# Optimization experiments

Measured on AMD Instinct MI355X. Metric: run time of the kernel, lower is better.

Reference implementation:

```python
import jax, jax.numpy as jnp
import numpy as np

N_BINS = 15
DELTA = 1.0 / N_BINS


def setup_inputs() -> dict:
    key = jax.random.key(0)
    k1, k2 = jax.random.split(key)
    N, C = 4_000_000, 10
    # scale 5 -> confident softmax -> low collision entropy so bins [0,1) are populated
    logits = jax.random.normal(k1, (N, C), dtype=jnp.float32) * 5.0
    labels = jax.random.randint(k2, (N,), 0, C)
    return {"logits": logits, "labels": labels}


def reference(logits, labels):
    # probs: [N, C]
    probs = jax.nn.softmax(logits, axis=-1)
    # collision entropy H2 per sample: [N]
    u = -jnp.log2(jnp.sum(probs * probs, axis=-1) + 1e-12)
    err_real = (jnp.argmax(probs, axis=-1) != labels).astype(jnp.float32)  # [N]

    n = u.shape[0]
    # bin b covers [b*DELTA, (b+1)*DELTA); samples with u outside [0,1) go to overflow bin
    bin_idx = jnp.floor(u / DELTA).astype(jnp.int32)
    valid = (u >= 0.0) & (u < 1.0)
    seg = jnp.where(valid, bin_idx, N_BINS)

    vf = valid.astype(jnp.float32)
    counts = jax.ops.segment_sum(vf, seg, num_segments=N_BINS + 1)[:N_BINS]
    sum_u = jax.ops.segment_sum(jnp.where(valid, u, 0.0), seg, num_segments=N_BINS + 1)[:N_BINS]
    sum_err = jax.ops.segment_sum(jnp.where(valid, err_real, 0.0), seg, num_segments=N_BINS + 1)[:N_BINS]

    pi = counts / n                      # population weight per bin
    nonempty = counts > 0
    cnt = jnp.where(nonempty, counts, 1.0)
    u_b = sum_u / cnt                    # mean H2 in bin
    err_b = sum_err / cnt                # empirical error rate in bin

    # risk-from-H2 reference curve
    inner = jnp.clip(2.0 * jnp.exp2(-u_b) - 1.0, 0.0, None)
    r_ref = 0.5 * (1.0 - jnp.sqrt(inner))

    gaps = jnp.where(nonempty, jnp.abs(err_b - r_ref) * pi, 0.0)
    return jnp.sum(gaps)
```

## Files before the change

### kernel.cpp

```cpp
#include <hip/hip_runtime.h>
#include <math.h>
#include <stdint.h>

#define NB 15
#define TROWS 512
#define TBYTES (TROWS * 40)
#define NCOPY 8
#define ACCSTRIDE 64


__device__ __forceinline__ void gload_lds16(const void* g, float* ldsBase, uint32_t ldsByteOff)
{
    __builtin_amdgcn_global_load_lds(
        (const __attribute__((address_space(1))) uint32_t*)g,
        (__attribute__((address_space(3))) uint32_t*)((char*)ldsBase + ldsByteOff),
        16, 0, 0);
}

__device__ __forceinline__ void row_stats(const float lv[10], float lvl_lab, bool rowOK,
                                          int& bin, float& u, int& e10)
{
    float m = lv[0];
#pragma unroll
    for (int j = 1; j < 10; ++j) m = fmaxf(m, lv[j]);

    const float c = 1.44269504088896340736f;
    float mc = m * c;
    float Z = 0.0f, S = 0.0f;
#pragma unroll
    for (int j = 0; j < 10; ++j) {
        float e = exp2f(fmaf(lv[j], c, -mc));
        Z += e;
        S = fmaf(e, e, S);
    }
    float ratio = S * __builtin_amdgcn_rcpf(Z * Z);
    u = -log2f(ratio + 1e-12f);

    bool valid = rowOK && (u >= 0.0f) && (u < 1.0f);
    bin = -1;
    if (valid) {
        bin = (int)(u * 15.0f);
        if (bin > 14) bin = 14;
    }
    if (!valid) u = 0.0f;
    e10 = (lvl_lab != m) ? 1 : 0;
}

__global__ __launch_bounds__(256) void bin_kernel(
    const float* __restrict__ logits,
    const int* __restrict__ labels,
    float* __restrict__ acc,
    int N, int numTiles)
{
    __shared__ float lds[TROWS * 10];
    __shared__ float s_acc[3 * NB];

    const int t = threadIdx.x;
    if (t < 3 * NB) s_acc[t] = 0.0f;
    const int wid  = t >> 6;
    const int lane = t & 63;

    int   pk[NB];
    float su[NB];
#pragma unroll
    for (int b = 0; b < NB; ++b) { pk[b] = 0; su[b] = 0.0f; }

    const char* srcB = (const char*)logits;
    const long long totB = (long long)N * 40;

    for (int tile = blockIdx.x; tile < numTiles; tile += gridDim.x) {
        const long long tb = (long long)tile * TBYTES;

        const int r0 = tile * TROWS + t;
        const int r1 = r0 + 256;
        const int lab0 = (r0 < N) ? labels[r0] : 0;
        const int lab1 = (r1 < N) ? labels[r1] : 0;

        __syncthreads();
#pragma unroll
        for (int k = 0; k < 5; ++k) {
            uint32_t loff = (uint32_t)(wid * 5 + k) << 10;
            long long gb = tb + loff + lane * 16;
            if (gb < totB)
                gload_lds16(srcB + gb, lds, __builtin_amdgcn_readfirstlane(loff));
        }
        __syncthreads();

        float a[10], b2[10];
        {
            const float2* p = (const float2*)(lds + t * 10);
#pragma unroll
            for (int j = 0; j < 5; ++j) { float2 w = p[j]; a[2*j] = w.x; a[2*j+1] = w.y; }
        }
        {
            const float2* p = (const float2*)(lds + (t + 256) * 10);
#pragma unroll
            for (int j = 0; j < 5; ++j) { float2 w = p[j]; b2[2*j] = w.x; b2[2*j+1] = w.y; }
        }
        float lvl0 = lds[t * 10 + lab0];
        float lvl1 = lds[(t + 256) * 10 + lab1];

        int binA, eA, binB, eB;
        float uA, uB;
        row_stats(a,  lvl0, r0 < N, binA, uA, eA);
        row_stats(b2, lvl1, r1 < N, binB, uB, eB);

        int incA = 1 + (eA << 16);
        int incB = 1 + (eB << 16);
#pragma unroll
        for (int b = 0; b < NB; ++b) {
            bool mA = (binA == b);
            bool mB = (binB == b);
            pk[b] += (mA ? incA : 0) + (mB ? incB : 0);
            su[b] += (mA ? uA : 0.0f) + (mB ? uB : 0.0f);
        }
    }

#pragma unroll
    for (int b = 0; b < NB; ++b) {
        int   p = pk[b];
        float s = su[b];
#pragma unroll
        for (int off = 1; off < 64; off <<= 1) {
            p += __shfl_xor(p, off, 64);
            s += __shfl_xor(s, off, 64);
        }
        if (lane == 0) {
            atomicAdd(&s_acc[b],          (float)(p & 0xFFFF));
            atomicAdd(&s_acc[NB + b],     s);
            atomicAdd(&s_acc[2 * NB + b], (float)(p >> 16));
        }
    }
    __syncthreads();
    if (t < 3 * NB) {
        float v = s_acc[t];
        if (v != 0.0f)
            atomicAdd(&acc[(blockIdx.x & (NCOPY - 1)) * ACCSTRIDE + t], v);
    }
}

__global__ void finalize_kernel(const float* __restrict__ acc,
                                float* __restrict__ out, float n)
{
    int b = threadIdx.x;
    float gap = 0.0f;
    if (b < NB) {
        float cnt = 0.0f, sumu = 0.0f, serr = 0.0f;
#pragma unroll
        for (int c = 0; c < NCOPY; ++c) {
            cnt  += acc[c * ACCSTRIDE + b];
            sumu += acc[c * ACCSTRIDE + NB + b];
            serr += acc[c * ACCSTRIDE + 2 * NB + b];
        }
        if (cnt > 0.0f) {
            float u_b   = sumu / cnt;
            float err_b = serr / cnt;
            float inner = 2.0f * exp2f(-u_b) - 1.0f;
            if (inner < 0.0f) inner = 0.0f;
            float r_ref = 0.5f * (1.0f - sqrtf(inner));
            gap = fabsf(err_b - r_ref) * (cnt / n);
        }
    }
#pragma unroll
    for (int off = 32; off >= 1; off >>= 1)
        gap += __shfl_xor(gap, off, 64);
    if (b == 0) out[0] = gap;
}

extern "C" void kernel_launch(void* const* d_in, const int* in_sizes, int n_in,
                              void* d_out, int out_size, void* d_ws, size_t ws_size,
                              hipStream_t stream)
{
    const float* logits = (const float*)d_in[0];
    const int*   labels = (const int*)d_in[1];
    const int N = in_sizes[1];

    float* acc = (float*)d_ws;
    hipMemsetAsync(acc, 0, NCOPY * ACCSTRIDE * sizeof(float), stream);

    const int numTiles = (N + TROWS - 1) / TROWS;
    int blocks = numTiles < 1792 ? numTiles : 1792;
    bin_kernel<<<blocks, 256, 0, stream>>>(logits, labels, acc, N, numTiles);
    finalize_kernel<<<1, 64, 0, stream>>>(acc, (float*)d_out, (float)N);
}
```

Measured before the change: 245.9 us.

## Double-buffer LDS tile loads and pack per-bin counters into nibbles

Adds a two-buffer LDS pipeline: the async global-to-LDS load for the next tile is issued before computing the current tile, and the label for the next tile is prefetched. This hides load latency and leaves one barrier per iteration. Tiles shrink to 256 rows, so each thread handles one row per iteration. The 15 packed int accumulators are replaced by four nibble-packed registers for counts and errors, which cuts register pressure. The catch is that each thread must see at most 15 rows per bin, which holds only while tiles per block stay below 16.

Result: no change. 248.5 us (+1.0%).

```diff
diff --git a/kernel.cpp b/kernel.cpp
--- a/kernel.cpp
+++ b/kernel.cpp
@@ -3,7 +3,7 @@
 #include <stdint.h>
 
 #define NB 15
-#define TROWS 512
+#define TROWS 256
 #define TBYTES (TROWS * 40)
 #define NCOPY 8
 #define ACCSTRIDE 64
@@ -17,42 +17,13 @@
         16, 0, 0);
 }
 
-__device__ __forceinline__ void row_stats(const float lv[10], float lvl_lab, bool rowOK,
-                                          int& bin, float& u, int& e10)
-{
-    float m = lv[0];
-#pragma unroll
-    for (int j = 1; j < 10; ++j) m = fmaxf(m, lv[j]);
-
-    const float c = 1.44269504088896340736f;
-    float mc = m * c;
-    float Z = 0.0f, S = 0.0f;
-#pragma unroll
-    for (int j = 0; j < 10; ++j) {
-        float e = exp2f(fmaf(lv[j], c, -mc));
-        Z += e;
-        S = fmaf(e, e, S);
-    }
-    float ratio = S * __builtin_amdgcn_rcpf(Z * Z);
-    u = -log2f(ratio + 1e-12f);
-
-    bool valid = rowOK && (u >= 0.0f) && (u < 1.0f);
-    bin = -1;
-    if (valid) {
-        bin = (int)(u * 15.0f);
-        if (bin > 14) bin = 14;
-    }
-    if (!valid) u = 0.0f;
-    e10 = (lvl_lab != m) ? 1 : 0;
-}
-
 __global__ __launch_bounds__(256) void bin_kernel(
     const float* __restrict__ logits,
     const int* __restrict__ labels,
     float* __restrict__ acc,
     int N, int numTiles)
 {
-    __shared__ float lds[TROWS * 10];
+    __shared__ float lds[2][TROWS * 10];
     __shared__ float s_acc[3 * NB];
 
     const int t = threadIdx.x;
@@ -60,65 +31,108 @@
     const int wid  = t >> 6;
     const int lane = t & 63;
 
-    int   pk[NB];
+    unsigned cnt01 = 0, cnt89 = 0, err01 = 0, err89 = 0;
     float su[NB];
 #pragma unroll
-    for (int b = 0; b < NB; ++b) { pk[b] = 0; su[b] = 0.0f; }
+    for (int b = 0; b < NB; ++b) su[b] = 0.0f;
 
     const char* srcB = (const char*)logits;
     const long long totB = (long long)N * 40;
+    const int k0 = wid, k1 = wid + 4, k2 = wid + 8;
 
-    for (int tile = blockIdx.x; tile < numTiles; tile += gridDim.x) {
+    int tile = blockIdx.x;
+    {
         const long long tb = (long long)tile * TBYTES;
+        long long gb0 = tb + (k0 << 10) + lane * 16;
+        long long gb1 = tb + (k1 << 10) + lane * 16;
+        if (gb0 < totB) gload_lds16(srcB + gb0, (float*)lds, __builtin_amdgcn_readfirstlane((uint32_t)(k0 << 10)));
+        if (gb1 < totB) gload_lds16(srcB + gb1, (float*)lds, __builtin_amdgcn_readfirstlane((uint32_t)(k1 << 10)));
+        if (k2 < 10) {
+            long long gb2 = tb + (k2 << 10) + lane * 16;
+            if (gb2 < totB) gload_lds16(srcB + gb2, (float*)lds, __builtin_amdgcn_readfirstlane((uint32_t)(k2 << 10)));
+        }
+    }
+    int r0 = tile * TROWS + t;
+    int labCur = (r0 < N) ? labels[r0] : 0;
 
-        const int r0 = tile * TROWS + t;
-        const int r1 = r0 + 256;
-        const int lab0 = (r0 < N) ? labels[r0] : 0;
-        const int lab1 = (r1 < N) ? labels[r1] : 0;
+    int cur = 0;
+    for (; tile < numTiles; tile += gridDim.x) {
+        const int nxt = tile + gridDim.x;
 
         __syncthreads();
+
+        int labNext = 0;
+        if (nxt < numTiles) {
+            const long long tb = (long long)nxt * TBYTES;
+            const uint32_t bufOff = (uint32_t)((cur ^ 1) * TBYTES);
+            long long gb0 = tb + (k0 << 10) + lane * 16;
+            long long gb1 = tb + (k1 << 10) + lane * 16;
+            if (gb0 < totB) gload_lds16(srcB + gb0, (float*)lds, __builtin_amdgcn_readfirstlane(bufOff + (k0 << 10)));
+            if (gb1 < totB) gload_lds16(srcB + gb1, (float*)lds, __builtin_amdgcn_readfirstlane(bufOff + (k1 << 10)));
+            if (k2 < 10) {
+                long long gb2 = tb + (k2 << 10) + lane * 16;
+                if (gb2 < totB) gload_lds16(srcB + gb2, (float*)lds, __builtin_amdgcn_readfirstlane(bufOff + (k2 << 10)));
+            }
+            int rn = nxt * TROWS + t;
+            labNext = (rn < N) ? labels[rn] : 0;
+        }
+
+        const int r = tile * TROWS + t;
+        const bool rowOK = (r < N);
+        const float* rp = lds[cur] + t * 10;
+        float lv[10];
+        {
+            const float2* p2 = (const float2*)rp;
 #pragma unroll
-        for (int k = 0; k < 5; ++k) {
-            uint32_t loff = (uint32_t)(wid * 5 + k) << 10;
-            long long gb = tb + loff + lane * 16;
-            if (gb < totB)
-                gload_lds16(srcB + gb, lds, __builtin_amdgcn_readfirstlane(loff));
+            for (int j = 0; j < 5; ++j) { float2 w = p2[j]; lv[2*j] = w.x; lv[2*j+1] = w.y; }
         }
-        __syncthreads();
+        float m = lv[0];
+#pragma unroll
+        for (int j = 1; j < 10; ++j) m = fmaxf(m, lv[j]);
 
-        float a[10], b2[10];
-        {
-            const float2* p = (const float2*)(lds + t * 10);
+        const float c = 1.44269504088896340736f;
+        float mc = m * c;
+        float Z = 0.0f, S = 0.0f;
 #pragma unroll
-            for (int j = 0; j < 5; ++j) { float2 w = p[j]; a[2*j] = w.x; a[2*j+1] = w.y; }
+        for (int j = 0; j < 10; ++j) {
+            float e = exp2f(fmaf(lv[j], c, -mc));
+            Z += e;
+            S = fmaf(e, e, S);
         }
-        {
-            const float2* p = (const float2*)(lds + (t + 256) * 10);
+        float ratio = S * __builtin_amdgcn_rcpf(Z * Z);
+        float u = -log2f(ratio + 1e-12f);
+
+        bool valid = rowOK && (u >= 0.0f) && (u < 1.0f);
+        int bin = -1;
+        if (valid) {
+            bin = (int)(u * 15.0f);
+            if (bin > 14) bin = 14;
+        }
+        float uu = valid ? u : 0.0f;
+
+        float lvl = rp[labCur];
+        bool e10 = (lvl != m);
+
+        unsigned nib = valid ? (1u << ((bin & 7) << 2)) : 0u;
+        bool lo = ((unsigned)bin < 8u);
+        cnt01 += lo ? nib : 0u;
+        cnt89 += lo ? 0u : nib;
+        unsigned en = e10 ? nib : 0u;
+        err01 += lo ? en : 0u;
+        err89 += lo ? 0u : en;
 #pragma unroll
-            for (int j = 0; j < 5; ++j) { float2 w = p[j]; b2[2*j] = w.x; b2[2*j+1] = w.y; }
-        }
-        float lvl0 = lds[t * 10 + lab0];
-        float lvl1 = lds[(t + 256) * 10 + lab1];
+        for (int b = 0; b < NB; ++b)
+            su[b] += (bin == b) ? uu : 0.0f;
 
-        int binA, eA, binB, eB;
-        float uA, uB;
-        row_stats(a,  lvl0, r0 < N, binA, uA, eA);
-        row_stats(b2, lvl1, r1 < N, binB, uB, eB);
-
-        int incA = 1 + (eA << 16);
-        int incB = 1 + (eB << 16);
-#pragma unroll
-        for (int b = 0; b < NB; ++b) {
-            bool mA = (binA == b);
-            bool mB = (binB == b);
-            pk[b] += (mA ? incA : 0) + (mB ? incB : 0);
-            su[b] += (mA ? uA : 0.0f) + (mB ? uB : 0.0f);
-        }
+        cur ^= 1;
+        labCur = labNext;
     }
 
 #pragma unroll
     for (int b = 0; b < NB; ++b) {
-        int   p = pk[b];
+        unsigned c4 = (b < 8) ? (cnt01 >> (b * 4)) : (cnt89 >> ((b - 8) * 4));
+        unsigned e4 = (b < 8) ? (err01 >> (b * 4)) : (err89 >> ((b - 8) * 4));
+        int   p = (int)((c4 & 15u) | ((e4 & 15u) << 16));
         float s = su[b];
 #pragma unroll
         for (int off = 1; off < 64; off <<= 1) {
@@ -128,7 +142,7 @@
         if (lane == 0) {
             atomicAdd(&s_acc[b],          (float)(p & 0xFFFF));
             atomicAdd(&s_acc[NB + b],     s);
-            atomicAdd(&s_acc[2 * NB + b], (float)(p >> 16));
+            atomicAdd(&s_acc[2 * NB + b], (float)((unsigned)p >> 16));
         }
     }
     __syncthreads();
```

## Double-buffer per-wave LDS DMA microtiles and pack bin counters into nibbles

Applied to the files above, without the earlier changes.

Replaces the block-wide tile loop, which needed two __syncthreads per tile, with independent per-wave 128-row microtiles. Each wave alternates between two LDS buffers: it issues the async global-to-LDS load and the label load for a later microtile while it computes on the current one. Bin counts and error counts now use 4-bit nibble counters in packed registers, and the grid is sized so each wave handles at most 15 microtiles, which keeps the nibbles from overflowing. The aim is to hide memory latency and cut synchronisation cost. In exchange, correctness depends on the compiler inserting the right vmcnt waits before LDS reads, and tails are handled with clamped loads.

Measured after the change: 246.5 us. About the same (+0.3%).

```diff
diff --git a/kernel.cpp b/kernel.cpp
--- a/kernel.cpp
+++ b/kernel.cpp
@@ -3,27 +3,48 @@
 #include <stdint.h>
 
 #define NB 15
-#define TROWS 512
-#define TBYTES (TROWS * 40)
 #define NCOPY 8
 #define ACCSTRIDE 64
 
 
-__device__ __forceinline__ void gload_lds16(const void* g, float* ldsBase, uint32_t ldsByteOff)
+__device__ __forceinline__ void dma16(const char* g, float* ldsArr, uint32_t byteOff)
 {
     __builtin_amdgcn_global_load_lds(
         (const __attribute__((address_space(1))) uint32_t*)g,
-        (__attribute__((address_space(3))) uint32_t*)((char*)ldsBase + ldsByteOff),
+        (__attribute__((address_space(3))) uint32_t*)((char*)ldsArr + byteOff),
         16, 0, 0);
 }
 
-__device__ __forceinline__ void row_stats(const float lv[10], float lvl_lab, bool rowOK,
-                                          int& bin, float& u, int& e10)
+__device__ __forceinline__ void stage_mt(const char* srcB, long long clampHi,
+                                         float* ldsArr, uint32_t segOff,
+                                         long long mClamped, int lane)
+{
+    long long g0 = mClamped * 5120 + (long long)lane * 16;
+#pragma unroll
+    for (int c = 0; c < 5; ++c) {
+        long long g = g0 + c * 1024;
+        g = (g > clampHi) ? clampHi : g;
+        dma16(srcB + g, ldsArr, segOff + (uint32_t)(c * 1024));
+    }
+}
+
+__device__ __forceinline__ void load_labs(const int* __restrict__ labels, long long mClamped,
+                                          int lane, int N, int& la0, int& la1)
+{
+    long long r0 = mClamped * 128 + lane;
+    long long r1 = r0 + 64;
+    r0 = (r0 < N) ? r0 : (N - 1);
+    r1 = (r1 < N) ? r1 : (N - 1);
+    la0 = labels[r0];
+    la1 = labels[r1];
+}
+
+__device__ __forceinline__ void row_math(const float lv[10], float lvl, bool rowOK,
+                                         int& bin, float& uu, bool& e10)
 {
     float m = lv[0];
 #pragma unroll
     for (int j = 1; j < 10; ++j) m = fmaxf(m, lv[j]);
-
     const float c = 1.44269504088896340736f;
     float mc = m * c;
     float Z = 0.0f, S = 0.0f;
@@ -34,91 +55,131 @@
         S = fmaf(e, e, S);
     }
     float ratio = S * __builtin_amdgcn_rcpf(Z * Z);
-    u = -log2f(ratio + 1e-12f);
-
+    float u = -log2f(ratio + 1e-12f);
     bool valid = rowOK && (u >= 0.0f) && (u < 1.0f);
     bin = -1;
     if (valid) {
         bin = (int)(u * 15.0f);
         if (bin > 14) bin = 14;
     }
-    if (!valid) u = 0.0f;
-    e10 = (lvl_lab != m) ? 1 : 0;
+    uu = valid ? u : 0.0f;
+    e10 = (lvl != m);
+}
+
+__device__ __forceinline__ void accum(int bin, float uu, bool e10,
+                                      unsigned& c01, unsigned& c89,
+                                      unsigned& e01, unsigned& e89, float su[NB])
+{
+    unsigned nib = (bin >= 0) ? (1u << ((bin & 7) << 2)) : 0u;
+    bool lo = ((unsigned)bin < 8u);
+    c01 += lo ? nib : 0u;
+    c89 += lo ? 0u : nib;
+    unsigned en = e10 ? nib : 0u;
+    e01 += lo ? en : 0u;
+    e89 += lo ? 0u : en;
+#pragma unroll
+    for (int b = 0; b < NB; ++b)
+        su[b] += (bin == b) ? uu : 0.0f;
+}
+
+__device__ __forceinline__ void consume_mt(const float* seg, int lane, long long kMT, int N,
+                                           int la0, int la1,
+                                           unsigned& c01a, unsigned& c89a, unsigned& e01a, unsigned& e89a,
+                                           unsigned& c01b, unsigned& c89b, unsigned& e01b, unsigned& e89b,
+                                           float su[NB])
+{
+    const float* r0p = seg + lane * 10;
+    const float* r1p = seg + (lane + 64) * 10;
+    float lv0[10], lv1[10];
+    {
+        const float2* p0 = (const float2*)r0p;
+        const float2* p1 = (const float2*)r1p;
+#pragma unroll
+        for (int j = 0; j < 5; ++j) {
+            float2 w0 = p0[j]; lv0[2*j] = w0.x; lv0[2*j+1] = w0.y;
+            float2 w1 = p1[j]; lv1[2*j] = w1.x; lv1[2*j+1] = w1.y;
+        }
+    }
+    float lvl0 = r0p[la0];
+    float lvl1 = r1p[la1];
+
+    long long r0 = kMT * 128 + lane;
+    bool ok0 = r0 < N;
+    bool ok1 = (r0 + 64) < N;
+
+    int bin0, bin1; float uu0, uu1; bool e0, e1;
+    row_math(lv0, lvl0, ok0, bin0, uu0, e0);
+    row_math(lv1, lvl1, ok1, bin1, uu1, e1);
+    accum(bin0, uu0, e0, c01a, c89a, e01a, e89a, su);
+    accum(bin1, uu1, e1, c01b, c89b, e01b, e89b, su);
 }
 
 __global__ __launch_bounds__(256) void bin_kernel(
     const float* __restrict__ logits,
     const int* __restrict__ labels,
     float* __restrict__ acc,
-    int N, int numTiles)
-{
-    __shared__ float lds[TROWS * 10];
+    int N, long long M, long long strideW)
+{
+    __shared__ float bufA[4 * 1280];
+    __shared__ float bufB[4 * 1280];
     __shared__ float s_acc[3 * NB];
 
     const int t = threadIdx.x;
     if (t < 3 * NB) s_acc[t] = 0.0f;
-    const int wid  = t >> 6;
-    const int lane = t & 63;
-
-    int   pk[NB];
-    float su[NB];
-#pragma unroll
-    for (int b = 0; b < NB; ++b) { pk[b] = 0; su[b] = 0.0f; }
-
+    __syncthreads();
+
+    const int wid = t >> 6, lane = t & 63;
+    const long long gw = (long long)blockIdx.x * 4 + wid;
     const char* srcB = (const char*)logits;
     const long long totB = (long long)N * 40;
-
-    for (int tile = blockIdx.x; tile < numTiles; tile += gridDim.x) {
-        const long long tb = (long long)tile * TBYTES;
-
-        const int r0 = tile * TROWS + t;
-        const int r1 = r0 + 256;
-        const int lab0 = (r0 < N) ? labels[r0] : 0;
-        const int lab1 = (r1 < N) ? labels[r1] : 0;
-
-        __syncthreads();
-#pragma unroll
-        for (int k = 0; k < 5; ++k) {
-            uint32_t loff = (uint32_t)(wid * 5 + k) << 10;
-            long long gb = tb + loff + lane * 16;
-            if (gb < totB)
-                gload_lds16(srcB + gb, lds, __builtin_amdgcn_readfirstlane(loff));
-        }
-        __syncthreads();
-
-        float a[10], b2[10];
-        {
-            const float2* p = (const float2*)(lds + t * 10);
-#pragma unroll
-            for (int j = 0; j < 5; ++j) { float2 w = p[j]; a[2*j] = w.x; a[2*j+1] = w.y; }
-        }
-        {
-            const float2* p = (const float2*)(lds + (t + 256) * 10);
-#pragma unroll
-            for (int j = 0; j < 5; ++j) { float2 w = p[j]; b2[2*j] = w.x; b2[2*j+1] = w.y; }
-        }
-        float lvl0 = lds[t * 10 + lab0];
-        float lvl1 = lds[(t + 256) * 10 + lab1];
-
-        int binA, eA, binB, eB;
-        float uA, uB;
-        row_stats(a,  lvl0, r0 < N, binA, uA, eA);
-        row_stats(b2, lvl1, r1 < N, binB, uB, eB);
-
-        int incA = 1 + (eA << 16);
-        int incB = 1 + (eB << 16);
-#pragma unroll
-        for (int b = 0; b < NB; ++b) {
-            bool mA = (binA == b);
-            bool mB = (binB == b);
-            pk[b] += (mA ? incA : 0) + (mB ? incB : 0);
-            su[b] += (mA ? uA : 0.0f) + (mB ? uB : 0.0f);
-        }
+    const long long clampHi = totB - 16;
+    const uint32_t segOff = __builtin_amdgcn_readfirstlane((uint32_t)(wid * 5120));
+    const float* segA = bufA + wid * 1280;
+    const float* segB = bufB + wid * 1280;
+
+    unsigned c01a = 0, c89a = 0, e01a = 0, e89a = 0;
+    unsigned c01b = 0, c89b = 0, e01b = 0, e89b = 0;
+    float su[NB];
+#pragma unroll
+    for (int b = 0; b < NB; ++b) su[b] = 0.0f;
+
+    long long mA = (gw < M) ? gw : (M - 1);
+    long long mBt = gw + strideW;
+    long long mB = (mBt < M) ? mBt : (M - 1);
+    int laA0, laA1, laB0, laB1;
+    stage_mt(srcB, clampHi, bufA, segOff, mA, lane);
+    load_labs(labels, mA, lane, N, laA0, laA1);
+    stage_mt(srcB, clampHi, bufB, segOff, mB, lane);
+    load_labs(labels, mB, lane, N, laB0, laB1);
+
+    long long k = gw;
+    while (k < M) {
+        consume_mt(segA, lane, k, N, laA0, laA1,
+                   c01a, c89a, e01a, e89a, c01b, c89b, e01b, e89b, su);
+        long long mA2 = k + 2 * strideW;
+        mA2 = (mA2 < M) ? mA2 : (M - 1);
+        stage_mt(srcB, clampHi, bufA, segOff, mA2, lane);
+        load_labs(labels, mA2, lane, N, laA0, laA1);
+
+        long long kB = k + strideW;
+        if (kB < M) {
+            consume_mt(segB, lane, kB, N, laB0, laB1,
+                       c01a, c89a, e01a, e89a, c01b, c89b, e01b, e89b, su);
+            long long mB2 = k + 3 * strideW;
+            mB2 = (mB2 < M) ? mB2 : (M - 1);
+            stage_mt(srcB, clampHi, bufB, segOff, mB2, lane);
+            load_labs(labels, mB2, lane, N, laB0, laB1);
+        }
+        k += 2 * strideW;
     }
 
 #pragma unroll
     for (int b = 0; b < NB; ++b) {
-        int   p = pk[b];
+        unsigned ca = (b < 8) ? (c01a >> (b * 4)) : (c89a >> ((b - 8) * 4));
+        unsigned cb = (b < 8) ? (c01b >> (b * 4)) : (c89b >> ((b - 8) * 4));
+        unsigned ea = (b < 8) ? (e01a >> (b * 4)) : (e89a >> ((b - 8) * 4));
+        unsigned eb = (b < 8) ? (e01b >> (b * 4)) : (e89b >> ((b - 8) * 4));
+        int   p = (int)(((ca & 15u) + (cb & 15u)) | (((ea & 15u) + (eb & 15u)) << 16));
         float s = su[b];
 #pragma unroll
         for (int off = 1; off < 64; off <<= 1) {
@@ -128,7 +189,7 @@
         if (lane == 0) {
             atomicAdd(&s_acc[b],          (float)(p & 0xFFFF));
             atomicAdd(&s_acc[NB + b],     s);
-            atomicAdd(&s_acc[2 * NB + b], (float)(p >> 16));
+            atomicAdd(&s_acc[2 * NB + b], (float)((unsigned)p >> 16));
         }
     }
     __syncthreads();
@@ -178,8 +239,15 @@
     float* acc = (float*)d_ws;
     hipMemsetAsync(acc, 0, NCOPY * ACCSTRIDE * sizeof(float), stream);
 
-    const int numTiles = (N + TROWS - 1) / TROWS;
-    int blocks = numTiles < 1792 ? numTiles : 1792;
-    bin_kernel<<<blocks, 256, 0, stream>>>(logits, labels, acc, N, numTiles);
+    const long long M = ((long long)N + 127) / 128;
+    int blocks = 768;
+    long long totW = (long long)blocks * 4;
+    long long mpw = (M + totW - 1) / totW;
+    if (mpw > 15) {
+        totW = (M + 14) / 15;
+        blocks = (int)((totW + 3) / 4);
+        totW = (long long)blocks * 4;
+    }
+    bin_kernel<<<blocks, 256, 0, stream>>>(logits, labels, acc, N, M, totW);
     finalize_kernel<<<1, 64, 0, stream>>>(acc, (float*)d_out, (float)N);
 }
```

## Fuse finalize into bin kernel via last-block counter and interleave row math

Applied to the files above, without the earlier changes.

Removes the separate finalize kernel launch by having the last block to finish, detected with a global atomic counter, compute the final gap reduction. The per-row statistics for the two rows are interleaved to expose more instruction-level parallelism. The LDS buffer is doubled but not used for double buffering, which may reduce occupancy. The error-count unpacking now uses an unsigned shift.

Measured after the change: 370.5 us. 1.51x slower.

```diff
diff --git a/kernel.cpp b/kernel.cpp
--- a/kernel.cpp
+++ b/kernel.cpp
@@ -17,43 +17,16 @@
         16, 0, 0);
 }
 
-__device__ __forceinline__ void row_stats(const float lv[10], float lvl_lab, bool rowOK,
-                                          int& bin, float& u, int& e10)
-{
-    float m = lv[0];
-#pragma unroll
-    for (int j = 1; j < 10; ++j) m = fmaxf(m, lv[j]);
-
-    const float c = 1.44269504088896340736f;
-    float mc = m * c;
-    float Z = 0.0f, S = 0.0f;
-#pragma unroll
-    for (int j = 0; j < 10; ++j) {
-        float e = exp2f(fmaf(lv[j], c, -mc));
-        Z += e;
-        S = fmaf(e, e, S);
-    }
-    float ratio = S * __builtin_amdgcn_rcpf(Z * Z);
-    u = -log2f(ratio + 1e-12f);
-
-    bool valid = rowOK && (u >= 0.0f) && (u < 1.0f);
-    bin = -1;
-    if (valid) {
-        bin = (int)(u * 15.0f);
-        if (bin > 14) bin = 14;
-    }
-    if (!valid) u = 0.0f;
-    e10 = (lvl_lab != m) ? 1 : 0;
-}
-
 __global__ __launch_bounds__(256) void bin_kernel(
     const float* __restrict__ logits,
     const int* __restrict__ labels,
     float* __restrict__ acc,
-    int N, int numTiles)
+    float* __restrict__ out,
+    int N, int numTiles, int nBlocks)
 {
-    __shared__ float lds[TROWS * 10];
+    __shared__ float lds[2 * TROWS * 10];
     __shared__ float s_acc[3 * NB];
+    __shared__ int   s_last;
 
     const int t = threadIdx.x;
     if (t < 3 * NB) s_acc[t] = 0.0f;
@@ -100,19 +73,45 @@
         float lvl0 = lds[t * 10 + lab0];
         float lvl1 = lds[(t + 256) * 10 + lab1];
 
-        int binA, eA, binB, eB;
-        float uA, uB;
-        row_stats(a,  lvl0, r0 < N, binA, uA, eA);
-        row_stats(b2, lvl1, r1 < N, binB, uB, eB);
+        const float c = 1.44269504088896340736f;
 
-        int incA = 1 + (eA << 16);
-        int incB = 1 + (eB << 16);
+        float mA = a[0];
+#pragma unroll
+        for (int j = 1; j < 10; ++j) mA = fmaxf(mA, a[j]);
+        float mB = b2[0];
+#pragma unroll
+        for (int j = 1; j < 10; ++j) mB = fmaxf(mB, b2[j]);
+
+        float mcA = mA * c, mcB = mB * c;
+        float ZA = 0.f, SA = 0.f, ZB = 0.f, SB = 0.f;
+#pragma unroll
+        for (int j = 0; j < 10; ++j) {
+            float eA = exp2f(fmaf(a[j],  c, -mcA));
+            float eB = exp2f(fmaf(b2[j], c, -mcB));
+            ZA += eA; SA = fmaf(eA, eA, SA);
+            ZB += eB; SB = fmaf(eB, eB, SB);
+        }
+        float uA = -log2f(SA * __builtin_amdgcn_rcpf(ZA * ZA) + 1e-12f);
+        float uB = -log2f(SB * __builtin_amdgcn_rcpf(ZB * ZB) + 1e-12f);
+
+        bool vA = (r0 < N) && (uA >= 0.0f) && (uA < 1.0f);
+        bool vB = (r1 < N) && (uB >= 0.0f) && (uB < 1.0f);
+        int binA = -1, binB = -1;
+        if (vA) { binA = (int)(uA * 15.0f); if (binA > 14) binA = 14; }
+        if (vB) { binB = (int)(uB * 15.0f); if (binB > 14) binB = 14; }
+        float uuA = vA ? uA : 0.0f;
+        float uuB = vB ? uB : 0.0f;
+
+        int eA10 = (lvl0 != mA) ? 1 : 0;
+        int eB10 = (lvl1 != mB) ? 1 : 0;
+        int incA = 1 + (eA10 << 16);
+        int incB = 1 + (eB10 << 16);
 #pragma unroll
         for (int b = 0; b < NB; ++b) {
-            bool mA = (binA == b);
-            bool mB = (binB == b);
-            pk[b] += (mA ? incA : 0) + (mB ? incB : 0);
-            su[b] += (mA ? uA : 0.0f) + (mB ? uB : 0.0f);
+            bool hA = (binA == b);
+            bool hB = (binB == b);
+            pk[b] += (hA ? incA : 0) + (hB ? incB : 0);
+            su[b] += (hA ? uuA : 0.0f) + (hB ? uuB : 0.0f);
         }
     }
 
@@ -128,7 +127,7 @@
         if (lane == 0) {
             atomicAdd(&s_acc[b],          (float)(p & 0xFFFF));
             atomicAdd(&s_acc[NB + b],     s);
-            atomicAdd(&s_acc[2 * NB + b], (float)(p >> 16));
+            atomicAdd(&s_acc[2 * NB + b], (float)((unsigned)p >> 16));
         }
     }
     __syncthreads();
@@ -137,34 +136,39 @@
         if (v != 0.0f)
             atomicAdd(&acc[(blockIdx.x & (NCOPY - 1)) * ACCSTRIDE + t], v);
     }
-}
 
-__global__ void finalize_kernel(const float* __restrict__ acc,
-                                float* __restrict__ out, float n)
-{
-    int b = threadIdx.x;
-    float gap = 0.0f;
-    if (b < NB) {
-        float cnt = 0.0f, sumu = 0.0f, serr = 0.0f;
+    __threadfence();
+    __syncthreads();
+    if (t == 0) {
+        int old = atomicAdd((int*)(acc + NCOPY * ACCSTRIDE), 1);
+        s_last = (old == nBlocks - 1) ? 1 : 0;
+    }
+    __syncthreads();
+    if (s_last && t < 64) {
+        int b = t;
+        float gap = 0.0f;
+        if (b < NB) {
+            float cnt = 0.0f, sumu = 0.0f, serr = 0.0f;
 #pragma unroll
-        for (int c = 0; c < NCOPY; ++c) {
-            cnt  += acc[c * ACCSTRIDE + b];
-            sumu += acc[c * ACCSTRIDE + NB + b];
-            serr += acc[c * ACCSTRIDE + 2 * NB + b];
+            for (int cc = 0; cc < NCOPY; ++cc) {
+                cnt  += atomicAdd(&acc[cc * ACCSTRIDE + b], 0.0f);
+                sumu += atomicAdd(&acc[cc * ACCSTRIDE + NB + b], 0.0f);
+                serr += atomicAdd(&acc[cc * ACCSTRIDE + 2 * NB + b], 0.0f);
+            }
+            if (cnt > 0.0f) {
+                float u_b   = sumu / cnt;
+                float err_b = serr / cnt;
+                float inner = 2.0f * exp2f(-u_b) - 1.0f;
+                if (inner < 0.0f) inner = 0.0f;
+                float r_ref = 0.5f * (1.0f - sqrtf(inner));
+                gap = fabsf(err_b - r_ref) * (cnt / (float)N);
+            }
         }
-        if (cnt > 0.0f) {
-            float u_b   = sumu / cnt;
-            float err_b = serr / cnt;
-            float inner = 2.0f * exp2f(-u_b) - 1.0f;
-            if (inner < 0.0f) inner = 0.0f;
-            float r_ref = 0.5f * (1.0f - sqrtf(inner));
-            gap = fabsf(err_b - r_ref) * (cnt / n);
-        }
+#pragma unroll
+        for (int off = 32; off >= 1; off >>= 1)
+            gap += __shfl_xor(gap, off, 64);
+        if (b == 0) out[0] = gap;
     }
-#pragma unroll
-    for (int off = 32; off >= 1; off >>= 1)
-        gap += __shfl_xor(gap, off, 64);
-    if (b == 0) out[0] = gap;
 }
 
 extern "C" void kernel_launch(void* const* d_in, const int* in_sizes, int n_in,
@@ -176,10 +180,10 @@
     const int N = in_sizes[1];
 
     float* acc = (float*)d_ws;
-    hipMemsetAsync(acc, 0, NCOPY * ACCSTRIDE * sizeof(float), stream);
+    hipMemsetAsync(acc, 0, (NCOPY * ACCSTRIDE + 1) * sizeof(float), stream);
 
     const int numTiles = (N + TROWS - 1) / TROWS;
     int blocks = numTiles < 1792 ? numTiles : 1792;
-    bin_kernel<<<blocks, 256, 0, stream>>>(logits, labels, acc, N, numTiles);
-    finalize_kernel<<<1, 64, 0, stream>>>(acc, (float*)d_out, (float)N);
+    bin_kernel<<<blocks, 256, 0, stream>>>(logits, labels, acc, (float*)d_out,
+                                           N, numTiles, blocks);
 }
```
